# Kernel tuning notes

Measured on AMD Instinct MI355X. Metric: run time of the kernel, lower is better.

## Reference

```python
import jax, jax.numpy as jnp
import numpy as np

# BEV volume configuration (module defaults)
W_RES, H_RES, D_RES = 100, 5, 100
WIDTH = (-10.0, 10.0)
HEIGHT = (-3.5, 1.5)
DEPTH = (0.0, 20.0)


def _span(lo, hi, n):
    step = (hi - lo) / n
    return jnp.linspace(lo + step / 2, hi - step / 2, n, dtype=jnp.float32)


def make_positions():
    # torch.meshgrid default indexing='ij'; stack (X,Y,Z) then flatten -> [N,3] -> T -> [3,N]
    wx = _span(WIDTH[0], WIDTH[1], W_RES)
    hy = _span(HEIGHT[0], HEIGHT[1], H_RES)
    dz = _span(DEPTH[0], DEPTH[1], D_RES)
    X, Y, Z = jnp.meshgrid(wx, hy, dz, indexing='ij')
    return jnp.stack([X, Y, Z], axis=3).reshape(-1, 3).T  # [3, N], N = W_RES*H_RES*D_RES


def grid_sample_bilinear(x, grid):
    """torch.nn.functional.grid_sample, mode='bilinear', align_corners=True, zero padding.
    x: [B,C,H,W], grid: [B,Hg,Wg,2] with (x,y) in [-1,1]. Returns [B,C,Hg,Wg]."""
    B, C, H, W = x.shape
    ix = (grid[..., 0] + 1.0) * 0.5 * (W - 1)  # align_corners=True mapping
    iy = (grid[..., 1] + 1.0) * 0.5 * (H - 1)
    ix0 = jnp.floor(ix)
    iy0 = jnp.floor(iy)

    def gather(xb, yi, xi):  # xb [C,H,W], yi/xi [Hg,Wg]
        return xb[:, yi, xi]  # [C,Hg,Wg]

    out = jnp.zeros((B, C) + grid.shape[1:3], dtype=x.dtype)
    for dy in (0, 1):
        for dx in (0, 1):
            xi = ix0 + dx
            yi = iy0 + dy
            w = (1.0 - jnp.abs(ix - xi)) * (1.0 - jnp.abs(iy - yi))  # bilinear weight
            valid = (xi >= 0) & (xi <= W - 1) & (yi >= 0) & (yi <= H - 1)
            w = jnp.where(valid, w, 0.0)
            xic = jnp.clip(xi, 0, W - 1).astype(jnp.int32)
            yic = jnp.clip(yi, 0, H - 1).astype(jnp.int32)
            v = jax.vmap(gather)(x, yic, xic)  # [B,C,Hg,Wg]
            out = out + v * w[:, None].astype(x.dtype)
    return out


def setup_inputs() -> dict:
    key = jax.random.key(0)
    k1, k2 = jax.random.split(key)
    X = jax.random.normal(k1, (4, 256, 96, 320), dtype=jnp.float32)
    # Pinhole-like normalized-intrinsics calib so most projected points land in [0,1]^2.
    K = jnp.array([[0.03, 0.0, 0.5], [0.0, 0.1, 0.5], [0.0, 0.0, 1.0]], dtype=jnp.float32)
    noise = jax.random.normal(k2, (4, 3, 3), dtype=jnp.float32) * 0.01
    noise = noise.at[:, 2, :].set(0.0)  # keep depth row exact to avoid z ~ 0
    calib = K[None] + noise
    return {"X": X, "calib": calib}


def reference(X, calib):
    bs, C = X.shape[0], X.shape[1]
    P = make_positions()  # [3, N]
    img = jnp.einsum('bij,jn->bin', calib, P)  # [B,3,N] per-batch projection
    z = img[:, 2:3, :]
    xy = 2.0 * (img[:, :2, :] / z - 0.5)  # normalized grid coords in [-1,1]
    grid = xy.transpose(0, 2, 1).reshape(bs, W_RES, H_RES * D_RES, 2)
    feat = grid_sample_bilinear(X, grid)  # [B,C,W_RES,H_RES*D_RES]
    feat = feat.reshape(bs, C, W_RES, H_RES, D_RES)
    feat = feat.transpose(0, 1, 3, 4, 2).reshape(bs, C * H_RES, D_RES, W_RES)
    return feat
```

## Files before the change

kernel.cpp:

```cpp
#include <hip/hip_runtime.h>


#define W_IN  320
#define H_IN  96
#define SLICE (H_IN * W_IN)
#define CG    16
#define NITEMS 50000

__global__ __launch_bounds__(256) void bev_kernel(const float* __restrict__ X,
                                                  const float* __restrict__ calib,
                                                  float* __restrict__ out) {
    const int bcg = blockIdx.y;
    const int b   = bcg >> 4;
    const int c0  = (bcg & 15) * CG;
    const int t   = blockIdx.x * 256 + threadIdx.x;
    if (t >= NITEMS) return;

    const int d = t / 500;
    const int r = t - d * 500;
    const int h = r / 100;
    const int w = r - h * 100;

    const float* cb = calib + b * 9;
    const float c00 = cb[0], c01 = cb[1], c02 = cb[2];
    const float c10 = cb[3], c11 = cb[4], c12 = cb[5];

    const float wxv = -9.9f + 0.2f * (float)w;
    const float hyv = -3.0f + (float)h;
    const float dzv = 0.1f + 0.2f * (float)d;
    const float inv = 1.0f / dzv;

    const float ix = 319.0f * inv * (c00 * wxv + c01 * hyv + c02 * dzv);
    const float iy =  95.0f * inv * (c10 * wxv + c11 * hyv + c12 * dzv);
    const float fx0 = floorf(ix), fy0 = floorf(iy);
    const int ix0 = (int)fx0, iy0 = (int)fy0;
    const float ax = ix - fx0, ay = iy - fy0;

    float a0, a1, b0, b1;
    if (ix0 >= 0 && ix0 <= 318)      { a0 = 1.0f - ax; a1 = ax; }
    else if (ix0 == -1)              { a0 = ax;        a1 = 0.0f; }
    else if (ix0 == 319)             { a0 = 0.0f;      a1 = 1.0f - ax; }
    else                             { a0 = 0.0f;      a1 = 0.0f; }
    if (iy0 >= 0 && iy0 <= 94)       { b0 = 1.0f - ay; b1 = ay; }
    else if (iy0 == -1)              { b0 = ay;        b1 = 0.0f; }
    else if (iy0 == 95)              { b0 = 0.0f;      b1 = 1.0f - ay; }
    else                             { b0 = 0.0f;      b1 = 0.0f; }

    const int xc = min(max(ix0, 0), 318);
    const int yc = min(max(iy0, 0), 94);
    const int off = yc * W_IN + xc;
    const float W00 = a0 * b0, W01 = a1 * b0, W10 = a0 * b1, W11 = a1 * b1;
    const float wsum = W00 + W01 + W10 + W11;

    const float* Xc = X + ((size_t)b * 256 + (size_t)c0) * SLICE + off;
    float* oc = out + ((size_t)b * 1280 + (size_t)c0 * 5 + (size_t)h) * 10000
                    + d * 100 + w;

    if (wsum > 0.0f) {
        float v00[CG], v01[CG], v10[CG], v11[CG];
        #pragma unroll
        for (int cc = 0; cc < CG; ++cc) {
            const float* p = Xc + (size_t)cc * SLICE;
            v00[cc] = p[0];
            v01[cc] = p[1];
            v10[cc] = p[320];
            v11[cc] = p[321];
        }
        #pragma unroll
        for (int cc = 0; cc < CG; ++cc) {
            float v = W00 * v00[cc];
            v = fmaf(W01, v01[cc], v);
            v = fmaf(W10, v10[cc], v);
            v = fmaf(W11, v11[cc], v);
            __builtin_nontemporal_store(v, oc + (size_t)cc * 50000);
        }
    } else {
        #pragma unroll
        for (int cc = 0; cc < CG; ++cc) {
            __builtin_nontemporal_store(0.0f, oc + (size_t)cc * 50000);
        }
    }
}

extern "C" void kernel_launch(void* const* d_in, const int* in_sizes, int n_in,
                              void* d_out, int out_size, void* d_ws, size_t ws_size,
                              hipStream_t stream) {
    const float* X     = (const float*)d_in[0];
    const float* calib = (const float*)d_in[1];
    float* out = (float*)d_out;

    dim3 grid((NITEMS + 255) / 256, 64);
    bev_kernel<<<grid, dim3(256), 0, stream>>>(X, calib, out);
}
```

Before: 82.30 us.

## Precompute sample offsets and weights once, then gather with smaller channel groups

```diff
diff --git a/kernel.cpp b/kernel.cpp
--- a/kernel.cpp
+++ b/kernel.cpp
@@ -4,17 +4,17 @@
 #define W_IN  320
 #define H_IN  96
 #define SLICE (H_IN * W_IN)
-#define CG    16
-#define NITEMS 50000
+#define NPOS  50000
+#define CG    4
 
-__global__ __launch_bounds__(256) void bev_kernel(const float* __restrict__ X,
-                                                  const float* __restrict__ calib,
-                                                  float* __restrict__ out) {
-    const int bcg = blockIdx.y;
-    const int b   = bcg >> 4;
-    const int c0  = (bcg & 15) * CG;
-    const int t   = blockIdx.x * 256 + threadIdx.x;
-    if (t >= NITEMS) return;
+typedef float f32x4 __attribute__((ext_vector_type(4)));
+
+__global__ __launch_bounds__(256) void coord_kernel(const float* __restrict__ calib,
+                                                    int2* __restrict__ offs,
+                                                    f32x4* __restrict__ wts) {
+    const int b = blockIdx.z;
+    const int t = blockIdx.x * 256 + threadIdx.x;
+    if (t >= NPOS) return;
 
     const int d = t / 500;
     const int r = t - d * 500;
@@ -48,15 +48,28 @@
 
     const int xc = min(max(ix0, 0), 318);
     const int yc = min(max(iy0, 0), 94);
-    const int off = yc * W_IN + xc;
-    const float W00 = a0 * b0, W01 = a1 * b0, W10 = a0 * b1, W11 = a1 * b1;
-    const float wsum = W00 + W01 + W10 + W11;
 
-    const float* Xc = X + ((size_t)b * 256 + (size_t)c0) * SLICE + off;
-    float* oc = out + ((size_t)b * 1280 + (size_t)c0 * 5 + (size_t)h) * 10000
-                    + d * 100 + w;
+    offs[b * NPOS + t] = make_int2(yc * W_IN + xc, h * 10000 + d * 100 + w);
+    f32x4 wv = { a0 * b0, a1 * b0, a0 * b1, a1 * b1 };
+    wts[b * NPOS + t] = wv;
+}
 
-    if (wsum > 0.0f) {
+__global__ __launch_bounds__(256) void gather_kernel(const float* __restrict__ X,
+                                                     const int2* __restrict__ offs,
+                                                     const f32x4* __restrict__ wts,
+                                                     float* __restrict__ out) {
+    const int b  = blockIdx.z;
+    const int c0 = blockIdx.y * CG;
+    const int t  = blockIdx.x * 256 + threadIdx.x;
+    if (t >= NPOS) return;
+
+    const int2  io = offs[b * NPOS + t];
+    const f32x4 wt = wts[b * NPOS + t];
+
+    const float* Xc = X + ((size_t)b * 256 + (size_t)c0) * SLICE + io.x;
+    float* oc = out + (size_t)b * 12800000 + (size_t)c0 * 50000 + io.y;
+
+    if (wt.x + wt.y + wt.z + wt.w > 0.0f) {
         float v00[CG], v01[CG], v10[CG], v11[CG];
         #pragma unroll
         for (int cc = 0; cc < CG; ++cc) {
@@ -68,10 +81,10 @@
         }
         #pragma unroll
         for (int cc = 0; cc < CG; ++cc) {
-            float v = W00 * v00[cc];
-            v = fmaf(W01, v01[cc], v);
-            v = fmaf(W10, v10[cc], v);
-            v = fmaf(W11, v11[cc], v);
+            float v = wt.x * v00[cc];
+            v = fmaf(wt.y, v01[cc], v);
+            v = fmaf(wt.z, v10[cc], v);
+            v = fmaf(wt.w, v11[cc], v);
             __builtin_nontemporal_store(v, oc + (size_t)cc * 50000);
         }
     } else {
@@ -89,6 +102,12 @@
     const float* calib = (const float*)d_in[1];
     float* out = (float*)d_out;
 
-    dim3 grid((NITEMS + 255) / 256, 64);
-    bev_kernel<<<grid, dim3(256), 0, stream>>>(X, calib, out);
+    int2*  offs = (int2*)d_ws;
+    f32x4* wts  = (f32x4*)((char*)d_ws + 4 * NPOS * sizeof(int2));
+
+    dim3 g1((NPOS + 255) / 256, 1, 4);
+    coord_kernel<<<g1, dim3(256), 0, stream>>>(calib, offs, wts);
+
+    dim3 g2((NPOS + 255) / 256, 256 / CG, 4);
+    gather_kernel<<<g2, dim3(256), 0, stream>>>(X, offs, wts, out);
 }
```

Result: slower. 88.64 us (+7.7%).
